# Kernel tuning notes

Measured on AMD Instinct MI355X. Metric: run time of the kernel, lower is better.

Reference implementation:

```python
import jax, jax.numpy as jnp
import numpy as np

DIM = 512
EPS = 1e-08
LN_EPS = 1e-05  # torch LayerNorm default


def layer_norm(x, g, b):
    mu = jnp.mean(x, axis=-1, keepdims=True)
    var = jnp.mean(jnp.square(x - mu), axis=-1, keepdims=True)
    return (x - mu) * jax.lax.rsqrt(var + LN_EPS) * g + b


def setup_inputs() -> dict:
    key = jax.random.key(0)
    ks = jax.random.split(key, 10)
    B, NQ, NK, D = 8, 1024, 2048, DIM
    s = 1.0 / np.sqrt(D)
    return {
        "inputs": jax.random.normal(ks[0], (B, NQ, D), jnp.float32),
        "context": jax.random.normal(ks[1], (B, NK, D), jnp.float32),
        "ln_in_g": jnp.ones((D,), jnp.float32),
        "ln_in_b": jnp.zeros((D,), jnp.float32),
        "ln_ctx_g": jnp.ones((D,), jnp.float32),
        "ln_ctx_b": jnp.zeros((D,), jnp.float32),
        "Wq": jax.random.uniform(ks[2], (D, D), jnp.float32, -s, s),
        "bq": jax.random.uniform(ks[3], (D,), jnp.float32, -s, s),
        "Wk": jax.random.uniform(ks[4], (D, D), jnp.float32, -s, s),
        "bk": jax.random.uniform(ks[5], (D,), jnp.float32, -s, s),
        "Wv": jax.random.uniform(ks[6], (D, D), jnp.float32, -s, s),
        "bv": jax.random.uniform(ks[7], (D,), jnp.float32, -s, s),
    }


def reference(inputs, context, ln_in_g, ln_in_b, ln_ctx_g, ln_ctx_b, Wq, bq, Wk, bk, Wv, bv):
    x = layer_norm(inputs, ln_in_g, ln_in_b)
    c = layer_norm(context, ln_ctx_g, ln_ctx_b)
    q = x @ Wq.T + bq  # [B, Nq, D]
    k = c @ Wk.T + bk  # [B, Nk, D]
    v = c @ Wv.T + bv  # [B, Nk, D]
    scale = DIM ** (-0.5)
    dots = jnp.einsum('bid,bjd->bij', q, k) * scale  # [B, Nq, Nk]
    attn = jax.nn.softmax(dots, axis=1) + EPS  # softmax over query axis
    attn = attn / jnp.sum(attn, axis=2, keepdims=True)  # renorm over key axis
    updates = jnp.einsum('bjd,bij->bid', v, attn)
    return updates
```

## Files before the change

### kernel.cpp

```cpp
#include <hip/hip_runtime.h>

using u16 = unsigned short;
typedef __attribute__((ext_vector_type(8))) short short8;
typedef __attribute__((ext_vector_type(4))) float floatx4;

#define NQ 1024
#define NK 2048
#define DD 512

__device__ __forceinline__ u16 f2bf(float f) {
  union { float f; unsigned u; } x; x.f = f;
  unsigned r = (x.u + 0x7fffu + ((x.u >> 16) & 1u)) >> 16;
  return (u16)r;
}
__device__ __forceinline__ float bf2f(u16 u) {
  union { unsigned u; float f; } x; x.u = ((unsigned)u) << 16; return x.f;
}
__device__ __forceinline__ float wave_sum(float v) {
#pragma unroll
  for (int off = 32; off > 0; off >>= 1) v += __shfl_down(v, off, 64);
  return v;
}
__device__ __forceinline__ void gload16(const u16* g, const u16* l) {
  __builtin_amdgcn_global_load_lds(
      (const __attribute__((address_space(1))) void*)g,
      (__attribute__((address_space(3))) void*)l, 16, 0, 0);
}

__global__ __launch_bounds__(256) void ln_prep(
    const float* __restrict__ X1, const float* __restrict__ G1,
    const float* __restrict__ B1, u16* __restrict__ Y1,
    const float* __restrict__ X2, const float* __restrict__ G2,
    const float* __restrict__ B2, u16* __restrict__ Y2,
    const float* __restrict__ Wq, const float* __restrict__ Wk,
    const float* __restrict__ Wv, u16* __restrict__ wqb,
    u16* __restrict__ wkb, u16* __restrict__ wvb, float* __restrict__ Zero) {
  int row = blockIdx.x;
  const int t = threadIdx.x;
  if (row >= 24576) {
    int bx = row - 24576;
    if (bx < 768) {
      const float* src = bx < 256 ? Wq : (bx < 512 ? Wk : Wv);
      u16* dst = bx < 256 ? wqb : (bx < 512 ? wkb : wvb);
      int i = ((bx & 255) * 256 + t) * 4;
      float4 v = *(const float4*)(src + i);
      ushort4 o;
      o.x = f2bf(v.x); o.y = f2bf(v.y); o.z = f2bf(v.z); o.w = f2bf(v.w);
      *(ushort4*)(dst + i) = o;
    } else {
      int i = ((bx - 768) * 256 + t) * 4;
      float4 z = {0.f, 0.f, 0.f, 0.f};
      *(float4*)(Zero + i) = z;
    }
    return;
  }
  const float *X, *G, *Bv; u16* Y;
  if (row < 8192) { X = X1; G = G1; Bv = B1; Y = Y1; }
  else { row -= 8192; X = X2; G = G2; Bv = B2; Y = Y2; }
  const float2 v = ((const float2*)(X + (long)row * DD))[t];
  float s = v.x + v.y, ss = v.x * v.x + v.y * v.y;
  __shared__ float red[8];
  float a = wave_sum(s), b = wave_sum(ss);
  if ((t & 63) == 0) { red[t >> 6] = a; red[4 + (t >> 6)] = b; }
  __syncthreads();
  float tot = red[0] + red[1] + red[2] + red[3];
  float tss = red[4] + red[5] + red[6] + red[7];
  float mu = tot * (1.f / DD);
  float var = tss * (1.f / DD) - mu * mu;
  float rs = rsqrtf(var + 1e-5f);
  float2 g2 = ((const float2*)G)[t];
  float2 b2 = ((const float2*)Bv)[t];
  ushort2 o;
  o.x = f2bf((v.x - mu) * rs * g2.x + b2.x);
  o.y = f2bf((v.y - mu) * rs * g2.y + b2.y);
  ((ushort2*)(Y + (long)row * DD))[t] = o;
}

__global__ __launch_bounds__(256) void gemm_bt(
    const u16* A, const u16* B, const float* bias, void* Cout,
    const u16* A2, const u16* B2, const float* bias2, void* Cout2,
    int K, long sAb, long sBb, long sCb, int ldC,
    float scale, int epi, float* aux0, const float* aux1) {
  __shared__ u16 lA[128 * 64];
  __shared__ u16 lB[128 * 64];
  __shared__ float colred[128];

  int m0, n0, bz;
  if (epi == 3) {
    bz = blockIdx.x; m0 = blockIdx.z * 128; n0 = blockIdx.y * 128;
  } else {
    bz = blockIdx.z; m0 = blockIdx.x * 128; n0 = blockIdx.y * 128;
    if (A2 != nullptr && blockIdx.x >= 64) {
      A = A2; B = B2; bias = bias2; Cout = Cout2;
      m0 = (blockIdx.x - 64) * 128;
    }
  }
  A += (long)bz * sAb;
  B += (long)bz * sBb;
  const int t = threadIdx.x, wave = t >> 6, lane = t & 63;
  const int fm = lane & 15, fq = lane >> 4;
  const int wm = (wave >> 1) * 64, wn = (wave & 1) * 64;

  const int srow = t >> 3;
  const int swz = ((t & 7) ^ (srow & 7)) * 8;
  const u16* gA = A + (long)(m0 + srow) * K + swz;
  const u16* gB = B + (long)(n0 + srow) * K + swz;
  const long gk32 = 32L * K;
  u16* dA = lA + wave * 512;
  u16* dB = lB + wave * 512;

  floatx4 acc[4][4];
#pragma unroll
  for (int x = 0; x < 4; ++x)
#pragma unroll
    for (int y = 0; y < 4; ++y) { floatx4 z = {0.f, 0.f, 0.f, 0.f}; acc[x][y] = z; }

  const int nkt = K >> 6;
  for (int kt = 0; kt < nkt; ++kt) {
    gload16(gA, dA);
    gload16(gA + gk32, dA + 2048);
    gload16(gA + 2 * gk32, dA + 4096);
    gload16(gA + 3 * gk32, dA + 6144);
    gload16(gB, dB);
    gload16(gB + gk32, dB + 2048);
    gload16(gB + 2 * gk32, dB + 4096);
    gload16(gB + 3 * gk32, dB + 6144);
    gA += 64; gB += 64;
    __syncthreads();
#pragma unroll
    for (int ks = 0; ks < 2; ++ks) {
      short8 af[4], bfr[4];
      const int csl = ((ks * 4 + fq) ^ (fm & 7)) * 8;
#pragma unroll
      for (int x = 0; x < 4; ++x)
        af[x] = *(const short8*)&lA[(wm + x * 16 + fm) * 64 + csl];
#pragma unroll
      for (int y = 0; y < 4; ++y)
        bfr[y] = *(const short8*)&lB[(wn + y * 16 + fm) * 64 + csl];
#pragma unroll
      for (int x = 0; x < 4; ++x)
#pragma unroll
        for (int y = 0; y < 4; ++y)
          acc[x][y] = __builtin_amdgcn_mfma_f32_16x16x32_bf16(af[x], bfr[y], acc[x][y], 0, 0, 0);
    }
    __syncthreads();
  }

  if (epi == 0) {
    float bs[4];
#pragma unroll
    for (int y = 0; y < 4; ++y) bs[y] = bias[n0 + wn + y * 16 + fm];
#pragma unroll
    for (int x = 0; x < 4; ++x)
#pragma unroll
      for (int y = 0; y < 4; ++y)
#pragma unroll
        for (int r = 0; r < 4; ++r) {
          int row = m0 + wm + x * 16 + fq * 4 + r;
          int col = n0 + wn + y * 16 + fm;
          ((u16*)Cout)[(long)bz * sCb + (long)row * ldC + col] =
              f2bf(acc[x][y][r] + bs[y]);
        }
  } else if (epi == 3) {
    float s4[4] = {0.f, 0.f, 0.f, 0.f};
#pragma unroll
    for (int x = 0; x < 4; ++x)
#pragma unroll
      for (int y = 0; y < 4; ++y)
#pragma unroll
        for (int r = 0; r < 4; ++r) {
          int row = m0 + wm + x * 16 + fq * 4 + r;
          int col = n0 + wn + y * 16 + fm;
          float e = __expf(acc[x][y][r] * scale);
          s4[y] += e;
          ((u16*)Cout)[(long)bz * sCb + (long)row * ldC + col] = f2bf(e);
        }
#pragma unroll
    for (int y = 0; y < 4; ++y) {
      s4[y] += __shfl_xor(s4[y], 16, 64);
      s4[y] += __shfl_xor(s4[y], 32, 64);
    }
    if (t < 128) colred[t] = 0.f;
    __syncthreads();
    if (fq == 0) {
#pragma unroll
      for (int y = 0; y < 4; ++y) atomicAdd(&colred[wn + y * 16 + fm], s4[y]);
    }
    __syncthreads();
    if (t < 128) atomicAdd(&aux0[bz * 2048 + n0 + t], colred[t]);
  } else {
    const int bb = n0 >> 11;
    const int j0c = n0 & 2047;
    float bsr[4][4];
#pragma unroll
    for (int x = 0; x < 4; ++x)
#pragma unroll
      for (int r = 0; r < 4; ++r)
        bsr[x][r] = bias[m0 + wm + x * 16 + fq * 4 + r];
    float izv[4];
#pragma unroll
    for (int y = 0; y < 4; ++y)
      izv[y] = __builtin_amdgcn_rcpf(aux1[bb * 2048 + j0c + wn + y * 16 + fm]);
    u16* Cg = (u16*)Cout + (long)bb * (512L * 2048) + j0c;
    float rs[4][4];
#pragma unroll
    for (int x = 0; x < 4; ++x)
#pragma unroll
      for (int r = 0; r < 4; ++r) rs[x][r] = 0.f;
#pragma unroll
    for (int x = 0; x < 4; ++x)
#pragma unroll
      for (int y = 0; y < 4; ++y)
#pragma unroll
        for (int r = 0; r < 4; ++r) {
          int rowd = m0 + wm + x * 16 + fq * 4 + r;
          int col = wn + y * 16 + fm;
          float val = acc[x][y][r] + bsr[x][r];
          rs[x][r] += val;
          Cg[(long)rowd * 2048 + col] = f2bf(val * izv[y]);
        }
#pragma unroll
    for (int x = 0; x < 4; ++x)
#pragma unroll
      for (int r = 0; r < 4; ++r) {
        float s = rs[x][r];
        s += __shfl_xor(s, 1, 64);
        s += __shfl_xor(s, 2, 64);
        s += __shfl_xor(s, 4, 64);
        s += __shfl_xor(s, 8, 64);
        if (fm == 0)
          atomicAdd(&aux0[bb * 512 + m0 + wm + x * 16 + fq * 4 + r], s);
      }
  }
}

__global__ __launch_bounds__(256) void rowsumR(const u16* __restrict__ E,
    const float* __restrict__ Z, float* __restrict__ invR) {
  const int row = blockIdx.x;
  const int b = row >> 10;
  const u16* p = E + (long)row * NK;
  const float* zp = Z + b * NK;
  const int t = threadIdx.x, j0 = t * 8;
  short8 v = *(const short8*)(p + j0);
  float4 z0 = *(const float4*)(zp + j0);
  float4 z1 = *(const float4*)(zp + j0 + 4);
  float sum = bf2f((u16)v[0]) * __builtin_amdgcn_rcpf(z0.x) +
              bf2f((u16)v[1]) * __builtin_amdgcn_rcpf(z0.y) +
              bf2f((u16)v[2]) * __builtin_amdgcn_rcpf(z0.z) +
              bf2f((u16)v[3]) * __builtin_amdgcn_rcpf(z0.w) +
              bf2f((u16)v[4]) * __builtin_amdgcn_rcpf(z1.x) +
              bf2f((u16)v[5]) * __builtin_amdgcn_rcpf(z1.y) +
              bf2f((u16)v[6]) * __builtin_amdgcn_rcpf(z1.z) +
              bf2f((u16)v[7]) * __builtin_amdgcn_rcpf(z1.w);
  __shared__ float red[4];
  float a = wave_sum(sum);
  if ((t & 63) == 0) red[t >> 6] = a;
  __syncthreads();
  if (t == 0) {
    float R = red[0] + red[1] + red[2] + red[3] + 2048.f * 1e-8f;
    invR[row] = 1.0f / R;
  }
}

__global__ __launch_bounds__(256) void gemm_pv(const u16* __restrict__ E,
    const u16* __restrict__ V, const float* __restrict__ colV,
    const float* __restrict__ invR, float* __restrict__ out) {
  __shared__ u16 lA[64 * 64];
  __shared__ u16 lB[64 * 64];
  const int b = blockIdx.z;
  const int m0 = blockIdx.x * 64, n0 = blockIdx.y * 64;
  const int t = threadIdx.x, wave = t >> 6, lane = t & 63;
  const int fm = lane & 15, fq = lane >> 4;
  const int wm = (wave >> 1) * 32, wn = (wave & 1) * 32;

  const int srow = t >> 3;
  const int swz = ((t & 7) ^ (srow & 7)) * 8;
  const u16* gA = E + (long)b * (1024L * 2048) + (long)(m0 + srow) * 2048 + swz;
  const u16* gB = V + (long)b * (512L * 2048) + (long)(n0 + srow) * 2048 + swz;
  u16* dA = lA + wave * 512;
  u16* dB = lB + wave * 512;

  floatx4 acc[2][2];
#pragma unroll
  for (int x = 0; x < 2; ++x)
#pragma unroll
    for (int y = 0; y < 2; ++y) { floatx4 z = {0.f, 0.f, 0.f, 0.f}; acc[x][y] = z; }

  for (int kt = 0; kt < 32; ++kt) {
    gload16(gA, dA);
    gload16(gA + 32L * 2048, dA + 2048);
    gload16(gB, dB);
    gload16(gB + 32L * 2048, dB + 2048);
    gA += 64; gB += 64;
    __syncthreads();
#pragma unroll
    for (int ks = 0; ks < 2; ++ks) {
      short8 af[2], bfr[2];
      const int csl = ((ks * 4 + fq) ^ (fm & 7)) * 8;
#pragma unroll
      for (int x = 0; x < 2; ++x)
        af[x] = *(const short8*)&lA[(wm + x * 16 + fm) * 64 + csl];
#pragma unroll
      for (int y = 0; y < 2; ++y)
        bfr[y] = *(const short8*)&lB[(wn + y * 16 + fm) * 64 + csl];
#pragma unroll
      for (int x = 0; x < 2; ++x)
#pragma unroll
        for (int y = 0; y < 2; ++y)
          acc[x][y] = __builtin_amdgcn_mfma_f32_16x16x32_bf16(af[x], bfr[y], acc[x][y], 0, 0, 0);
    }
    __syncthreads();
  }

  float cv[2], ir[8];
#pragma unroll
  for (int y = 0; y < 2; ++y) cv[y] = colV[b * 512 + n0 + wn + y * 16 + fm];
#pragma unroll
  for (int x = 0; x < 2; ++x)
#pragma unroll
    for (int r = 0; r < 4; ++r)
      ir[x * 4 + r] = invR[b * 1024 + m0 + wm + x * 16 + fq * 4 + r];
  float* og = out + (long)b * (1024L * 512);
#pragma unroll
  for (int x = 0; x < 2; ++x)
#pragma unroll
    for (int y = 0; y < 2; ++y)
#pragma unroll
      for (int r = 0; r < 4; ++r) {
        int row = m0 + wm + x * 16 + fq * 4 + r;
        int col = n0 + wn + y * 16 + fm;
        og[(long)row * 512 + col] =
            (acc[x][y][r] + 1e-8f * cv[y]) * ir[x * 4 + r];
      }
}

extern "C" void kernel_launch(void* const* d_in, const int* in_sizes, int n_in,
                              void* d_out, int out_size, void* d_ws, size_t ws_size,
                              hipStream_t stream) {
  const float* inputs  = (const float*)d_in[0];
  const float* context = (const float*)d_in[1];
  const float* ln_in_g = (const float*)d_in[2];
  const float* ln_in_b = (const float*)d_in[3];
  const float* ln_ctx_g = (const float*)d_in[4];
  const float* ln_ctx_b = (const float*)d_in[5];
  const float* Wq = (const float*)d_in[6];
  const float* bq = (const float*)d_in[7];
  const float* Wk = (const float*)d_in[8];
  const float* bk = (const float*)d_in[9];
  const float* Wv = (const float*)d_in[10];
  const float* bv = (const float*)d_in[11];
  float* out = (float*)d_out;

  u16* ws = (u16*)d_ws;
  u16* xb  = ws;
  u16* qb  = xb + 8192L * 512;
  u16* cb  = qb + 8192L * 512;
  u16* wqb = cb + 16384L * 512;
  u16* wkb = wqb + 512L * 512;
  u16* wvb = wkb + 512L * 512;
  u16* kb  = wvb + 512L * 512;
  u16* vTs = kb + 16384L * 512;
  u16* E   = vTs + 8L * 512 * 2048;
  float* Z    = (float*)(E + 8L * 1024 * 2048);
  float* colV = Z + 8L * 2048;
  float* invR = colV + 8L * 512;

  const float scale = 0.04419417382415922f;

  ln_prep<<<25364, 256, 0, stream>>>(inputs, ln_in_g, ln_in_b, xb,
                                     context, ln_ctx_g, ln_ctx_b, cb,
                                     Wq, Wk, Wv, wqb, wkb, wvb, Z);
  gemm_bt<<<dim3(192, 4, 1), 256, 0, stream>>>(xb, wqb, bq, qb,
      cb, wkb, bk, kb, 512, 0L, 0L, 0L, 512, 1.0f, 0, nullptr, nullptr);
  gemm_bt<<<dim3(8, 16, 8), 256, 0, stream>>>(qb, kb, nullptr, E,
      nullptr, nullptr, nullptr, nullptr,
      512, 1024L * 512, 2048L * 512, 1024L * 2048, 2048, scale, 3, Z, nullptr);
  gemm_bt<<<dim3(4, 128, 1), 256, 0, stream>>>(wvb, cb, bv, vTs,
      nullptr, nullptr, nullptr, nullptr,
      512, 0L, 0L, 0L, 2048, 1.0f, 6, colV, Z);
  rowsumR<<<8192, 256, 0, stream>>>(E, Z, invR);
  gemm_pv<<<dim3(16, 8, 8), 256, 0, stream>>>(E, vTs, colV, invR, out);
}
```

Measured before the change: 230.5 us.

## Fuse row-sum normalization into PV GEMM via extra MFMA against 1/Z vector

Removes the separate rowsumR kernel that reread the full E matrix to compute the per-row renormalization. Each PV block now stages 1/Z as bf16 in shared memory and runs one extra MFMA per row fragment, so the row sums accumulate alongside the main product. The reciprocal is taken in the epilogue. This saves a full pass over E and a launch, in exchange for about 50% more MFMA work in gemm_pv (one extra per four), some LDS, and bf16 rounding of 1/Z.

```diff
diff --git a/kernel.cpp b/kernel.cpp
--- a/kernel.cpp
+++ b/kernel.cpp
@@ -234,44 +234,33 @@
   }
 }
 
-__global__ __launch_bounds__(256) void rowsumR(const u16* __restrict__ E,
-    const float* __restrict__ Z, float* __restrict__ invR) {
-  const int row = blockIdx.x;
-  const int b = row >> 10;
-  const u16* p = E + (long)row * NK;
-  const float* zp = Z + b * NK;
-  const int t = threadIdx.x, j0 = t * 8;
-  short8 v = *(const short8*)(p + j0);
-  float4 z0 = *(const float4*)(zp + j0);
-  float4 z1 = *(const float4*)(zp + j0 + 4);
-  float sum = bf2f((u16)v[0]) * __builtin_amdgcn_rcpf(z0.x) +
-              bf2f((u16)v[1]) * __builtin_amdgcn_rcpf(z0.y) +
-              bf2f((u16)v[2]) * __builtin_amdgcn_rcpf(z0.z) +
-              bf2f((u16)v[3]) * __builtin_amdgcn_rcpf(z0.w) +
-              bf2f((u16)v[4]) * __builtin_amdgcn_rcpf(z1.x) +
-              bf2f((u16)v[5]) * __builtin_amdgcn_rcpf(z1.y) +
-              bf2f((u16)v[6]) * __builtin_amdgcn_rcpf(z1.z) +
-              bf2f((u16)v[7]) * __builtin_amdgcn_rcpf(z1.w);
-  __shared__ float red[4];
-  float a = wave_sum(sum);
-  if ((t & 63) == 0) red[t >> 6] = a;
-  __syncthreads();
-  if (t == 0) {
-    float R = red[0] + red[1] + red[2] + red[3] + 2048.f * 1e-8f;
-    invR[row] = 1.0f / R;
-  }
-}
-
 __global__ __launch_bounds__(256) void gemm_pv(const u16* __restrict__ E,
     const u16* __restrict__ V, const float* __restrict__ colV,
-    const float* __restrict__ invR, float* __restrict__ out) {
+    const float* __restrict__ Z, float* __restrict__ out) {
   __shared__ u16 lA[64 * 64];
   __shared__ u16 lB[64 * 64];
+  __shared__ u16 sZb[2048];
   const int b = blockIdx.z;
   const int m0 = blockIdx.x * 64, n0 = blockIdx.y * 64;
   const int t = threadIdx.x, wave = t >> 6, lane = t & 63;
   const int fm = lane & 15, fq = lane >> 4;
   const int wm = (wave >> 1) * 32, wn = (wave & 1) * 32;
+
+  {
+    int i = t * 8;
+    float4 z0 = *(const float4*)(Z + b * 2048 + i);
+    float4 z1 = *(const float4*)(Z + b * 2048 + i + 4);
+    short8 o;
+    o[0] = (short)f2bf(__builtin_amdgcn_rcpf(z0.x));
+    o[1] = (short)f2bf(__builtin_amdgcn_rcpf(z0.y));
+    o[2] = (short)f2bf(__builtin_amdgcn_rcpf(z0.z));
+    o[3] = (short)f2bf(__builtin_amdgcn_rcpf(z0.w));
+    o[4] = (short)f2bf(__builtin_amdgcn_rcpf(z1.x));
+    o[5] = (short)f2bf(__builtin_amdgcn_rcpf(z1.y));
+    o[6] = (short)f2bf(__builtin_amdgcn_rcpf(z1.z));
+    o[7] = (short)f2bf(__builtin_amdgcn_rcpf(z1.w));
+    *(short8*)&sZb[i] = o;
+  }
 
   const int srow = t >> 3;
   const int swz = ((t & 7) ^ (srow & 7)) * 8;
@@ -281,10 +270,14 @@
   u16* dB = lB + wave * 512;
 
   floatx4 acc[2][2];
-#pragma unroll
-  for (int x = 0; x < 2; ++x)
-#pragma unroll
-    for (int y = 0; y < 2; ++y) { floatx4 z = {0.f, 0.f, 0.f, 0.f}; acc[x][y] = z; }
+  floatx4 accR[2];
+#pragma unroll
+  for (int x = 0; x < 2; ++x) {
+    floatx4 z = {0.f, 0.f, 0.f, 0.f};
+    accR[x] = z;
+#pragma unroll
+    for (int y = 0; y < 2; ++y) acc[x][y] = z;
+  }
 
   for (int kt = 0; kt < 32; ++kt) {
     gload16(gA, dA);
@@ -296,42 +289,42 @@
 #pragma unroll
     for (int ks = 0; ks < 2; ++ks) {
       short8 af[2], bfr[2];
-      const int csl = ((ks * 4 + fq) ^ (fm & 7)) * 8;
+      const int chunk = ks * 4 + fq;
+      const int csl = (chunk ^ (fm & 7)) * 8;
 #pragma unroll
       for (int x = 0; x < 2; ++x)
         af[x] = *(const short8*)&lA[(wm + x * 16 + fm) * 64 + csl];
 #pragma unroll
       for (int y = 0; y < 2; ++y)
         bfr[y] = *(const short8*)&lB[(wn + y * 16 + fm) * 64 + csl];
-#pragma unroll
-      for (int x = 0; x < 2; ++x)
+      short8 zf = *(const short8*)&sZb[kt * 64 + chunk * 8];
+#pragma unroll
+      for (int x = 0; x < 2; ++x) {
 #pragma unroll
         for (int y = 0; y < 2; ++y)
           acc[x][y] = __builtin_amdgcn_mfma_f32_16x16x32_bf16(af[x], bfr[y], acc[x][y], 0, 0, 0);
-    }
-    __syncthreads();
-  }
-
-  float cv[2], ir[8];
+        accR[x] = __builtin_amdgcn_mfma_f32_16x16x32_bf16(af[x], zf, accR[x], 0, 0, 0);
+      }
+    }
+    __syncthreads();
+  }
+
+  float cv[2];
 #pragma unroll
   for (int y = 0; y < 2; ++y) cv[y] = colV[b * 512 + n0 + wn + y * 16 + fm];
+  float* og = out + (long)b * (1024L * 512);
 #pragma unroll
   for (int x = 0; x < 2; ++x)
 #pragma unroll
-    for (int r = 0; r < 4; ++r)
-      ir[x * 4 + r] = invR[b * 1024 + m0 + wm + x * 16 + fq * 4 + r];
-  float* og = out + (long)b * (1024L * 512);
-#pragma unroll
-  for (int x = 0; x < 2; ++x)
-#pragma unroll
-    for (int y = 0; y < 2; ++y)
-#pragma unroll
-      for (int r = 0; r < 4; ++r) {
-        int row = m0 + wm + x * 16 + fq * 4 + r;
+    for (int r = 0; r < 4; ++r) {
+      float invR = __builtin_amdgcn_rcpf(accR[x][r] + 2048.f * 1e-8f);
+      int row = m0 + wm + x * 16 + fq * 4 + r;
+#pragma unroll
+      for (int y = 0; y < 2; ++y) {
         int col = n0 + wn + y * 16 + fm;
-        og[(long)row * 512 + col] =
-            (acc[x][y][r] + 1e-8f * cv[y]) * ir[x * 4 + r];
+        og[(long)row * 512 + col] = (acc[x][y][r] + 1e-8f * cv[y]) * invR;
       }
+    }
 }
 
 extern "C" void kernel_launch(void* const* d_in, const int* in_sizes, int n_in,
@@ -363,7 +356,6 @@
   u16* E   = vTs + 8L * 512 * 2048;
   float* Z    = (float*)(E + 8L * 1024 * 2048);
   float* colV = Z + 8L * 2048;
-  float* invR = colV + 8L * 512;
 
   const float scale = 0.04419417382415922f;
 
@@ -378,6 +370,5 @@
   gemm_bt<<<dim3(4, 128, 1), 256, 0, stream>>>(wvb, cb, bv, vTs,
       nullptr, nullptr, nullptr, nullptr,
       512, 0L, 0L, 0L, 2048, 1.0f, 6, colV, Z);
-  rowsumR<<<8192, 256, 0, stream>>>(E, Z, invR);
-  gemm_pv<<<dim3(16, 8, 8), 256, 0, stream>>>(E, vTs, colV, invR, out);
-}
+  gemm_pv<<<dim3(16, 8, 8), 256, 0, stream>>>(E, vTs, colV, Z, out);
+}
```

Result: faster. 224.6 us (-2.6%).
